# Kernel optimization log

Measured on AMD Instinct MI355X. Metric: run time of the kernel, lower is better.

The kernel has to match this reference:

```python
import jax, jax.numpy as jnp
import numpy as np

N, K, D = 32768, 1024, 512


def setup_inputs() -> dict:
    key = jax.random.key(0)
    kf, kc = jax.random.split(key)
    features = jax.random.normal(kf, (N, D), dtype=jnp.float32)
    centers = jax.random.normal(kc, (K, D), dtype=jnp.float32)
    return {"features": features, "centers": centers}


def reference(features, centers):
    # m = 2 => exponent 2/(m-1) = 2, so sum(|x - c|**2, dim=2) is a squared
    # Euclidean distance. Compute it via the GEMM identity
    x2 = jnp.sum(features * features, axis=1, keepdims=True)          # [N, 1]
    c2 = jnp.sum(centers * centers, axis=1)                           # [K]
    d = x2 - 2.0 * (features @ centers.T) + c2                        # [N, K]
    inv = 1.0 / d                                                     # mu = 1 / sum(|x-c|^2)
    mu = inv / jnp.sum(inv, axis=1, keepdims=True)                    # normalize over K
    return mu


if __name__ == "__main__":
    out = reference(**setup_inputs())
    print(out.shape, out.dtype)
```

## Files before the change

kernel.cpp:

```cpp
#include <hip/hip_runtime.h>
#include <hip/hip_bf16.h>
#include <stdint.h>

#define N_ROWS 32768
#define K_CENT 1024
#define D_DIM  512

typedef __attribute__((ext_vector_type(8))) short bf16x8;
typedef __attribute__((ext_vector_type(4))) float f32x4;
typedef __attribute__((ext_vector_type(8))) unsigned short u16x8;

__device__ unsigned short g_cbT[K_CENT * D_DIM];
__device__ float          g_c2[K_CENT];

static __device__ __forceinline__ unsigned short f2bf(float x) {
    unsigned u = __float_as_uint(x);
    return (unsigned short)((u + 0x7FFFu + ((u >> 16) & 1u)) >> 16);
}

__global__ __launch_bounds__(64) void prep_centers(const float* __restrict__ centers) {
    const int row = blockIdx.x;
    const int s   = threadIdx.x;
    const float4 v0 = *reinterpret_cast<const float4*>(centers + (size_t)row * D_DIM + s * 8);
    const float4 v1 = *reinterpret_cast<const float4*>(centers + (size_t)row * D_DIM + s * 8 + 4);
    float sq = v0.x * v0.x + v0.y * v0.y + v0.z * v0.z + v0.w * v0.w
             + v1.x * v1.x + v1.y * v1.y + v1.z * v1.z + v1.w * v1.w;
    u16x8 pk;
    pk[0] = f2bf(v0.x); pk[1] = f2bf(v0.y); pk[2] = f2bf(v0.z); pk[3] = f2bf(v0.w);
    pk[4] = f2bf(v1.x); pk[5] = f2bf(v1.y); pk[6] = f2bf(v1.z); pk[7] = f2bf(v1.w);
    const int h  = row >> 9;
    const int rc = (row >> 6) & 7;
    const int l  = row & 63;
    const int k  = s >> 2;
    const int ds = s & 3;
    const size_t off = ((size_t)(((h * 16 + k) * 32) + ds * 8 + rc) * 64 + l) * 8;
    *reinterpret_cast<u16x8*>(g_cbT + off) = pk;
    #pragma unroll
    for (int m = 1; m < 64; m <<= 1) sq += __shfl_xor(sq, m);
    if (s == 0) g_c2[row] = sq;
}

static __device__ __forceinline__ void stageB(unsigned short* bbuf, int w, int l,
                                              int k, int half) {
    #pragma unroll
    for (int j = 0; j < 4; ++j) {
        const int p = w * 4 + j;
        unsigned short* ldst = bbuf + (size_t)p * 512;
        const unsigned short* gsrc =
            g_cbT + ((size_t)(((half * 16 + k) * 32) + p)) * 512 + l * 8;
        __builtin_amdgcn_global_load_lds(
            (const __attribute__((address_space(1))) void*)gsrc,
            (__attribute__((address_space(3))) void*)ldst, 16, 0, 0);
    }
}

static __device__ __forceinline__ void compute_half(const unsigned short* A_lds,
                                                    const unsigned short* bbuf,
                                                    int k, int w, int l15, int l4,
                                                    f32x4 (&acc)[4][4]) {
    bf16x8 a[4], b[4];
    #pragma unroll
    for (int mi = 0; mi < 4; ++mi)
        a[mi] = *reinterpret_cast<const bf16x8*>(
            &A_lds[((size_t)((k * 4 + l4) * 64 + mi * 16 + l15)) * 8]);
    #pragma unroll
    for (int ni = 0; ni < 4; ++ni)
        b[ni] = *reinterpret_cast<const bf16x8*>(
            &bbuf[((size_t)(l4 * 512 + w * 64 + ni * 16 + l15)) * 8]);
    #pragma unroll
    for (int mi = 0; mi < 4; ++mi)
        #pragma unroll
        for (int ni = 0; ni < 4; ++ni)
            acc[mi][ni] = __builtin_amdgcn_mfma_f32_16x16x32_bf16(a[mi], b[ni],
                                                                  acc[mi][ni], 0, 0, 0);
}

__global__ __launch_bounds__(512, 2) void fuzzy_mu_kernel(const float* __restrict__ feats,
                                                          float* __restrict__ out) {
    __shared__ unsigned short A_lds[64 * 64 * 8];
    __shared__ unsigned short B_lds[2][4 * 512 * 8];
    __shared__ float x2s[64];
    __shared__ float rs[64];

    const int tid = threadIdx.x;
    const int l   = tid & 63;
    const int w   = tid >> 6;
    const int l15 = l & 15;
    const int l4  = l >> 4;

    const int bid  = blockIdx.x;
    const int bswz = (bid & 7) * 64 + (bid >> 3);
    const int nb   = bswz * 64;

    if (tid < 64) { rs[tid] = 0.0f; }

    {
        const int row = tid >> 3;
        const int s   = tid & 7;
        const float* src = feats + (size_t)(nb + row) * D_DIM;
        float sq = 0.f;
        #pragma unroll
        for (int j = 0; j < 8; ++j) {
            const int c0 = s * 64 + j * 8;
            const float4 v0 = *reinterpret_cast<const float4*>(src + c0);
            const float4 v1 = *reinterpret_cast<const float4*>(src + c0 + 4);
            sq += v0.x * v0.x + v0.y * v0.y + v0.z * v0.z + v0.w * v0.w;
            sq += v1.x * v1.x + v1.y * v1.y + v1.z * v1.z + v1.w * v1.w;
            u16x8 pk;
            pk[0] = f2bf(v0.x); pk[1] = f2bf(v0.y); pk[2] = f2bf(v0.z); pk[3] = f2bf(v0.w);
            pk[4] = f2bf(v1.x); pk[5] = f2bf(v1.y); pk[6] = f2bf(v1.z); pk[7] = f2bf(v1.w);
            const int ds = s * 8 + j;
            *reinterpret_cast<u16x8*>(&A_lds[((size_t)(ds * 64 + row)) * 8]) = pk;
        }
        sq += __shfl_xor(sq, 1);
        sq += __shfl_xor(sq, 2);
        sq += __shfl_xor(sq, 4);
        if (s == 0) x2s[row] = sq;
    }

    f32x4 acc0[4][4], acc1[4][4];
    const f32x4 zz = {0.f, 0.f, 0.f, 0.f};
    #pragma unroll
    for (int mi = 0; mi < 4; ++mi)
        #pragma unroll
        for (int ni = 0; ni < 4; ++ni) { acc0[mi][ni] = zz; acc1[mi][ni] = zz; }

    stageB(B_lds[0], w, l, 0, 0);
    __syncthreads();

    for (int k = 0; k < 16; ++k) {
        stageB(B_lds[1], w, l, k, 1);
        compute_half(A_lds, B_lds[0], k, w, l15, l4, acc0);
        __syncthreads();

        if (k < 15) stageB(B_lds[0], w, l, k + 1, 0);
        compute_half(A_lds, B_lds[1], k, w, l15, l4, acc1);
        __syncthreads();
    }

    float rowpart[4][4];
    #pragma unroll
    for (int mi = 0; mi < 4; ++mi)
        #pragma unroll
        for (int j = 0; j < 4; ++j) rowpart[mi][j] = 0.f;

    #pragma unroll
    for (int mi = 0; mi < 4; ++mi) {
        #pragma unroll
        for (int ni = 0; ni < 4; ++ni) {
            const int cb  = w * 64 + ni * 16 + l15;
            const float c2v0 = g_c2[cb];
            const float c2v1 = g_c2[512 + cb];
            #pragma unroll
            for (int j = 0; j < 4; ++j) {
                const float xv = x2s[mi * 16 + l4 * 4 + j];
                const float d0 = xv - 2.f * acc0[mi][ni][j] + c2v0;
                const float d1 = xv - 2.f * acc1[mi][ni][j] + c2v1;
                const float i0 = 1.f / d0;
                const float i1 = 1.f / d1;
                acc0[mi][ni][j] = i0;
                acc1[mi][ni][j] = i1;
                rowpart[mi][j] += i0 + i1;
            }
        }
    }
    #pragma unroll
    for (int mi = 0; mi < 4; ++mi) {
        #pragma unroll
        for (int j = 0; j < 4; ++j) {
            float v = rowpart[mi][j];
            v += __shfl_xor(v, 1);
            v += __shfl_xor(v, 2);
            v += __shfl_xor(v, 4);
            v += __shfl_xor(v, 8);
            if (l15 == 0) atomicAdd(&rs[mi * 16 + l4 * 4 + j], v);
        }
    }
    __syncthreads();

    #pragma unroll
    for (int mi = 0; mi < 4; ++mi) {
        #pragma unroll
        for (int j = 0; j < 4; ++j) {
            const int rl = mi * 16 + l4 * 4 + j;
            const float rinv = 1.0f / rs[rl];
            float* op = out + (size_t)(nb + rl) * K_CENT + w * 64 + l15;
            #pragma unroll
            for (int ni = 0; ni < 4; ++ni) {
                op[ni * 16]       = acc0[mi][ni][j] * rinv;
                op[512 + ni * 16] = acc1[mi][ni][j] * rinv;
            }
        }
    }
}

extern "C" void kernel_launch(void* const* d_in, const int* in_sizes, int n_in,
                              void* d_out, int out_size, void* d_ws, size_t ws_size,
                              hipStream_t stream) {
    const float* feats = (const float*)d_in[0];
    const float* cents = (const float*)d_in[1];
    float* out = (float*)d_out;

    prep_centers<<<K_CENT, 64, 0, stream>>>(cents);
    fuzzy_mu_kernel<<<N_ROWS / 64, 512, 0, stream>>>(feats, out);
}
```

Measured before the change: 249.3 us.

## Load B fragments directly from global in MFMA layout, use 1024-thread blocks

Centers are pre-packed in prep_centers into the exact per-lane MFMA fragment order, so the main kernel loads B operands straight from global memory (L2) into registers. This removes the LDS double-buffer staging and the per-iteration barriers. Blocks grow to 16 waves so each wave owns one 64-column slice of the 1024 centers with a single accumulator set. The trade-off is that B now comes from L2/global memory each iteration with no LDS reuse or explicit prefetch, and occupancy changes with the larger blocks.

Result: faster. 221.9 us (-11.0%).

```diff
diff --git a/kernel.cpp b/kernel.cpp
--- a/kernel.cpp
+++ b/kernel.cpp
@@ -10,7 +10,7 @@
 typedef __attribute__((ext_vector_type(4))) float f32x4;
 typedef __attribute__((ext_vector_type(8))) unsigned short u16x8;
 
-__device__ unsigned short g_cbT[K_CENT * D_DIM];
+__device__ unsigned short g_cbF[K_CENT * D_DIM];
 __device__ float          g_c2[K_CENT];
 
 static __device__ __forceinline__ unsigned short f2bf(float x) {
@@ -28,57 +28,22 @@
     u16x8 pk;
     pk[0] = f2bf(v0.x); pk[1] = f2bf(v0.y); pk[2] = f2bf(v0.z); pk[3] = f2bf(v0.w);
     pk[4] = f2bf(v1.x); pk[5] = f2bf(v1.y); pk[6] = f2bf(v1.z); pk[7] = f2bf(v1.w);
-    const int h  = row >> 9;
-    const int rc = (row >> 6) & 7;
-    const int l  = row & 63;
-    const int k  = s >> 2;
-    const int ds = s & 3;
-    const size_t off = ((size_t)(((h * 16 + k) * 32) + ds * 8 + rc) * 64 + l) * 8;
-    *reinterpret_cast<u16x8*>(g_cbT + off) = pk;
+    const int k   = s >> 2;
+    const int l4  = s & 3;
+    const int w   = row >> 6;
+    const int ni  = (row >> 4) & 3;
+    const int l15 = row & 15;
+    const int l   = l4 * 16 + l15;
+    const size_t off = ((size_t)(((k * 16 + w) * 4 + ni) * 64 + l)) * 8;
+    *reinterpret_cast<u16x8*>(g_cbF + off) = pk;
     #pragma unroll
     for (int m = 1; m < 64; m <<= 1) sq += __shfl_xor(sq, m);
     if (s == 0) g_c2[row] = sq;
 }
 
-static __device__ __forceinline__ void stageB(unsigned short* bbuf, int w, int l,
-                                              int k, int half) {
-    #pragma unroll
-    for (int j = 0; j < 4; ++j) {
-        const int p = w * 4 + j;
-        unsigned short* ldst = bbuf + (size_t)p * 512;
-        const unsigned short* gsrc =
-            g_cbT + ((size_t)(((half * 16 + k) * 32) + p)) * 512 + l * 8;
-        __builtin_amdgcn_global_load_lds(
-            (const __attribute__((address_space(1))) void*)gsrc,
-            (__attribute__((address_space(3))) void*)ldst, 16, 0, 0);
-    }
-}
-
-static __device__ __forceinline__ void compute_half(const unsigned short* A_lds,
-                                                    const unsigned short* bbuf,
-                                                    int k, int w, int l15, int l4,
-                                                    f32x4 (&acc)[4][4]) {
-    bf16x8 a[4], b[4];
-    #pragma unroll
-    for (int mi = 0; mi < 4; ++mi)
-        a[mi] = *reinterpret_cast<const bf16x8*>(
-            &A_lds[((size_t)((k * 4 + l4) * 64 + mi * 16 + l15)) * 8]);
-    #pragma unroll
-    for (int ni = 0; ni < 4; ++ni)
-        b[ni] = *reinterpret_cast<const bf16x8*>(
-            &bbuf[((size_t)(l4 * 512 + w * 64 + ni * 16 + l15)) * 8]);
-    #pragma unroll
-    for (int mi = 0; mi < 4; ++mi)
-        #pragma unroll
-        for (int ni = 0; ni < 4; ++ni)
-            acc[mi][ni] = __builtin_amdgcn_mfma_f32_16x16x32_bf16(a[mi], b[ni],
-                                                                  acc[mi][ni], 0, 0, 0);
-}
-
-__global__ __launch_bounds__(512, 2) void fuzzy_mu_kernel(const float* __restrict__ feats,
-                                                          float* __restrict__ out) {
+__global__ __launch_bounds__(1024) void fuzzy_mu_kernel(const float* __restrict__ feats,
+                                                        float* __restrict__ out) {
     __shared__ unsigned short A_lds[64 * 64 * 8];
-    __shared__ unsigned short B_lds[2][4 * 512 * 8];
     __shared__ float x2s[64];
     __shared__ float rs[64];
 
@@ -92,16 +57,16 @@
     const int bswz = (bid & 7) * 64 + (bid >> 3);
     const int nb   = bswz * 64;
 
-    if (tid < 64) { rs[tid] = 0.0f; }
+    if (tid < 64) rs[tid] = 0.0f;
 
     {
-        const int row = tid >> 3;
-        const int s   = tid & 7;
+        const int row = tid >> 4;
+        const int s   = tid & 15;
         const float* src = feats + (size_t)(nb + row) * D_DIM;
         float sq = 0.f;
         #pragma unroll
-        for (int j = 0; j < 8; ++j) {
-            const int c0 = s * 64 + j * 8;
+        for (int j = 0; j < 4; ++j) {
+            const int c0 = s * 32 + j * 8;
             const float4 v0 = *reinterpret_cast<const float4*>(src + c0);
             const float4 v1 = *reinterpret_cast<const float4*>(src + c0 + 4);
             sq += v0.x * v0.x + v0.y * v0.y + v0.z * v0.z + v0.w * v0.w;
@@ -109,33 +74,43 @@
             u16x8 pk;
             pk[0] = f2bf(v0.x); pk[1] = f2bf(v0.y); pk[2] = f2bf(v0.z); pk[3] = f2bf(v0.w);
             pk[4] = f2bf(v1.x); pk[5] = f2bf(v1.y); pk[6] = f2bf(v1.z); pk[7] = f2bf(v1.w);
-            const int ds = s * 8 + j;
+            const int ds = s * 4 + j;
             *reinterpret_cast<u16x8*>(&A_lds[((size_t)(ds * 64 + row)) * 8]) = pk;
         }
         sq += __shfl_xor(sq, 1);
         sq += __shfl_xor(sq, 2);
         sq += __shfl_xor(sq, 4);
+        sq += __shfl_xor(sq, 8);
         if (s == 0) x2s[row] = sq;
     }
 
-    f32x4 acc0[4][4], acc1[4][4];
+    f32x4 acc[4][4];
     const f32x4 zz = {0.f, 0.f, 0.f, 0.f};
     #pragma unroll
     for (int mi = 0; mi < 4; ++mi)
         #pragma unroll
-        for (int ni = 0; ni < 4; ++ni) { acc0[mi][ni] = zz; acc1[mi][ni] = zz; }
+        for (int ni = 0; ni < 4; ++ni) acc[mi][ni] = zz;
 
-    stageB(B_lds[0], w, l, 0, 0);
     __syncthreads();
 
+    #pragma unroll 2
     for (int k = 0; k < 16; ++k) {
-        stageB(B_lds[1], w, l, k, 1);
-        compute_half(A_lds, B_lds[0], k, w, l15, l4, acc0);
-        __syncthreads();
-
-        if (k < 15) stageB(B_lds[0], w, l, k + 1, 0);
-        compute_half(A_lds, B_lds[1], k, w, l15, l4, acc1);
-        __syncthreads();
+        const unsigned short* bb = g_cbF + ((size_t)(k * 16 + w) * 4) * 512 + l * 8;
+        bf16x8 b[4];
+        #pragma unroll
+        for (int ni = 0; ni < 4; ++ni)
+            b[ni] = *reinterpret_cast<const bf16x8*>(bb + ni * 512);
+        bf16x8 a[4];
+        #pragma unroll
+        for (int mi = 0; mi < 4; ++mi)
+            a[mi] = *reinterpret_cast<const bf16x8*>(
+                &A_lds[((size_t)((k * 4 + l4) * 64 + mi * 16 + l15)) * 8]);
+        #pragma unroll
+        for (int mi = 0; mi < 4; ++mi)
+            #pragma unroll
+            for (int ni = 0; ni < 4; ++ni)
+                acc[mi][ni] = __builtin_amdgcn_mfma_f32_16x16x32_bf16(a[mi], b[ni],
+                                                                      acc[mi][ni], 0, 0, 0);
     }
 
     float rowpart[4][4];
@@ -148,19 +123,14 @@
     for (int mi = 0; mi < 4; ++mi) {
         #pragma unroll
         for (int ni = 0; ni < 4; ++ni) {
-            const int cb  = w * 64 + ni * 16 + l15;
-            const float c2v0 = g_c2[cb];
-            const float c2v1 = g_c2[512 + cb];
+            const float c2v = g_c2[w * 64 + ni * 16 + l15];
             #pragma unroll
             for (int j = 0; j < 4; ++j) {
                 const float xv = x2s[mi * 16 + l4 * 4 + j];
-                const float d0 = xv - 2.f * acc0[mi][ni][j] + c2v0;
-                const float d1 = xv - 2.f * acc1[mi][ni][j] + c2v1;
-                const float i0 = 1.f / d0;
-                const float i1 = 1.f / d1;
-                acc0[mi][ni][j] = i0;
-                acc1[mi][ni][j] = i1;
-                rowpart[mi][j] += i0 + i1;
+                const float dd = xv - 2.f * acc[mi][ni][j] + c2v;
+                const float iv = 1.f / dd;
+                acc[mi][ni][j] = iv;
+                rowpart[mi][j] += iv;
             }
         }
     }
@@ -186,10 +156,8 @@
             const float rinv = 1.0f / rs[rl];
             float* op = out + (size_t)(nb + rl) * K_CENT + w * 64 + l15;
             #pragma unroll
-            for (int ni = 0; ni < 4; ++ni) {
-                op[ni * 16]       = acc0[mi][ni][j] * rinv;
-                op[512 + ni * 16] = acc1[mi][ni][j] * rinv;
-            }
+            for (int ni = 0; ni < 4; ++ni)
+                op[ni * 16] = acc[mi][ni][j] * rinv;
         }
     }
 }
@@ -202,5 +170,5 @@
     float* out = (float*)d_out;
 
     prep_centers<<<K_CENT, 64, 0, stream>>>(cents);
-    fuzzy_mu_kernel<<<N_ROWS / 64, 512, 0, stream>>>(feats, out);
+    fuzzy_mu_kernel<<<N_ROWS / 64, 1024, 0, stream>>>(feats, out);
 }
```
